# Optimization experiments

Measured on AMD Instinct MI355X. Metric: run time of the kernel, lower is better.

The kernel has to match this reference:

```python
import jax, jax.numpy as jnp
import numpy as np

NUM_BASES = 8


def setup_inputs() -> dict:
    key = jax.random.key(0)
    ks = jax.random.split(key, 8)
    N, E = 100000, 1600000
    IN_F, OUT_F, NUM_RELS = 128, 128, 16
    si = IN_F // NUM_BASES   # 16
    so = OUT_F // NUM_BASES  # 16
    return {
        "h": jax.random.normal(ks[0], (N, IN_F), dtype=jnp.float32),
        "norm": jax.random.uniform(ks[1], (N, 1), dtype=jnp.float32),
        "edge_src": jax.random.randint(ks[2], (E,), 0, N, dtype=jnp.int32),
        "edge_dst": jax.random.randint(ks[3], (E,), 0, N, dtype=jnp.int32),
        "edge_type": jax.random.randint(ks[4], (E,), 0, NUM_RELS, dtype=jnp.int32),
        "weight": jax.random.normal(ks[5], (NUM_RELS, NUM_BASES * si * so), dtype=jnp.float32) * 0.1,
        "bias_param": jax.random.normal(ks[6], (OUT_F,), dtype=jnp.float32) * 0.1,
        "loop_weight": jax.random.normal(ks[7], (IN_F, OUT_F), dtype=jnp.float32) * 0.1,
    }


def reference(h, norm, edge_src, edge_dst, edge_type, weight, bias_param, loop_weight):
    N, in_feat = h.shape
    out_feat = loop_weight.shape[1]
    si = in_feat // NUM_BASES
    so = out_feat // NUM_BASES
    E = edge_type.shape[0]

    # self-loop message (dropout=0.0 -> identity)
    loop_message = h @ loop_weight                      # [N, out_feat]

    # msg_func: gather per-edge relation weight blocks and do block-diag bmm
    W = weight[edge_type].reshape(E, NUM_BASES, si, so)  # [E, B, si, so]
    src = h[edge_src].reshape(E, NUM_BASES, si)          # [E, B, si]
    msg = jnp.einsum("ebi,ebio->ebo", src, W).reshape(E, out_feat)

    # scatter-sum messages to destination nodes, rescale by norm
    agg = jax.ops.segment_sum(msg, edge_dst, num_segments=N)  # [N, out_feat]
    node_repr = agg * norm

    # bias + self-loop + activation
    node_repr = node_repr + bias_param + loop_message
    return jax.nn.relu(node_repr)
```

## Files before the change

kernel.cpp:

```cpp
#include <hip/hip_runtime.h>


__global__ __launch_bounds__(256) void rgcn_init_kernel(
    const float* __restrict__ h, const float* __restrict__ loop_w,
    const float* __restrict__ bias, float* __restrict__ out, int N) {
  __shared__ float lw[128 * 128];
  for (int idx = threadIdx.x; idx < 128 * 128 / 4; idx += 256) {
    ((float4*)lw)[idx] = ((const float4*)loop_w)[idx];
  }
  __syncthreads();

  const int lane = threadIdx.x & 63;
  const int wid = threadIdx.x >> 6;
  const int group0 = blockIdx.x * 4 + wid;
  const int ngroups = gridDim.x * 4;
  const int totgroups = (N + 3) >> 2;
  const float b0 = bias[lane];
  const float b1 = bias[64 + lane];

  for (int g = group0; g < totgroups; g += ngroups) {
    const int n0 = g * 4;
    const int nn = (N - n0 < 4) ? (N - n0) : 4;
    if (nn == 4) {
      const float* __restrict__ r0 = h + (size_t)n0 * 128;
      const float* __restrict__ r1 = r0 + 128;
      const float* __restrict__ r2 = r1 + 128;
      const float* __restrict__ r3 = r2 + 128;
      float a00 = b0, a01 = b1, a10 = b0, a11 = b1;
      float a20 = b0, a21 = b1, a30 = b0, a31 = b1;
#pragma unroll 4
      for (int k = 0; k < 128; ++k) {
        const float w0 = lw[k * 128 + lane];
        const float w1 = lw[k * 128 + 64 + lane];
        a00 = fmaf(r0[k], w0, a00); a01 = fmaf(r0[k], w1, a01);
        a10 = fmaf(r1[k], w0, a10); a11 = fmaf(r1[k], w1, a11);
        a20 = fmaf(r2[k], w0, a20); a21 = fmaf(r2[k], w1, a21);
        a30 = fmaf(r3[k], w0, a30); a31 = fmaf(r3[k], w1, a31);
      }
      float* __restrict__ o0 = out + (size_t)n0 * 128;
      o0[lane] = a00;        o0[64 + lane] = a01;
      o0[128 + lane] = a10;  o0[192 + lane] = a11;
      o0[256 + lane] = a20;  o0[320 + lane] = a21;
      o0[384 + lane] = a30;  o0[448 + lane] = a31;
    } else {
      for (int r = 0; r < nn; ++r) {
        const int n = n0 + r;
        const float* __restrict__ hr = h + (size_t)n * 128;
        float a0 = b0, a1 = b1;
#pragma unroll 4
        for (int k = 0; k < 128; ++k) {
          const float a = hr[k];
          a0 = fmaf(a, lw[k * 128 + lane], a0);
          a1 = fmaf(a, lw[k * 128 + 64 + lane], a1);
        }
        out[(size_t)n * 128 + lane] = a0;
        out[(size_t)n * 128 + 64 + lane] = a1;
      }
    }
  }
}

__global__ __launch_bounds__(256) void rgcn_edge_kernel(
    const float* __restrict__ h, const float* __restrict__ norm,
    const int* __restrict__ esrc, const int* __restrict__ edst,
    const int* __restrict__ etype, const float* __restrict__ weight,
    float* __restrict__ out, int E) {
  const int lane = threadIdx.x & 63;
  const int wid = threadIdx.x >> 6;
  const int wave0 = blockIdx.x * 4 + wid;
  const int nwaves = gridDim.x * 4;
  const int b = lane >> 4;
  const int o = lane & 15;

  for (int e = wave0; e < E; e += nwaves) {
    const int src = esrc[e];
    const int dst = edst[e];
    const int et = etype[e];

    const float s_lo = h[src * 128 + lane];
    const float s_hi = h[src * 128 + 64 + lane];
    const float nrm = norm[dst];

    const float* __restrict__ Wb = weight + et * 2048 + b * 256 + o;

    float m0 = 0.f, m1 = 0.f;
#pragma unroll
    for (int i = 0; i < 16; ++i) {
      const float a_lo = __shfl(s_lo, (lane & 48) + i, 64);
      const float a_hi = __shfl(s_hi, (lane & 48) + i, 64);
      m0 = fmaf(a_lo, Wb[i * 16], m0);
      m1 = fmaf(a_hi, Wb[1024 + i * 16], m1);
    }

    atomicAdd(&out[dst * 128 + lane], m0 * nrm);
    atomicAdd(&out[dst * 128 + 64 + lane], m1 * nrm);
  }
}

__global__ __launch_bounds__(256) void rgcn_relu_kernel(float* __restrict__ out,
                                                        int total4) {
  int i = blockIdx.x * 256 + threadIdx.x;
  const int stride = gridDim.x * 256;
  for (; i < total4; i += stride) {
    float4 v = ((float4*)out)[i];
    v.x = fmaxf(v.x, 0.f);
    v.y = fmaxf(v.y, 0.f);
    v.z = fmaxf(v.z, 0.f);
    v.w = fmaxf(v.w, 0.f);
    ((float4*)out)[i] = v;
  }
}

extern "C" void kernel_launch(void* const* d_in, const int* in_sizes, int n_in,
                              void* d_out, int out_size, void* d_ws, size_t ws_size,
                              hipStream_t stream) {
  const float* h      = (const float*)d_in[0];
  const float* norm   = (const float*)d_in[1];
  const int*   esrc   = (const int*)d_in[2];
  const int*   edst   = (const int*)d_in[3];
  const int*   etype  = (const int*)d_in[4];
  const float* weight = (const float*)d_in[5];
  const float* bias   = (const float*)d_in[6];
  const float* loop_w = (const float*)d_in[7];
  float* out = (float*)d_out;

  const int N = in_sizes[0] / 128;
  const int E = in_sizes[2];

  rgcn_init_kernel<<<2048, 256, 0, stream>>>(h, loop_w, bias, out, N);
  rgcn_edge_kernel<<<4096, 256, 0, stream>>>(h, norm, esrc, edst, etype, weight,
                                             out, E);
  rgcn_relu_kernel<<<2048, 256, 0, stream>>>(out, (N * 128) / 4);
}
```

Baseline: 927.8 us.

## Bucket edges by relation type and cache relation weights in registers per wave

Adds a counting-sort pipeline (histogram, scan, scatter) that groups edges by relation type into workspace buffers. A new edge kernel then gives each wave a contiguous chunk of sorted edges and reloads the 32 per-lane relation weights only when the type changes, replacing the shuffles with float4 loads of the source row. This cuts repeated weight gathers per edge at the cost of extra sort passes and 12 bytes of workspace traffic per edge. It falls back to the old kernel when the workspace is too small.

```diff
diff --git a/kernel.cpp b/kernel.cpp
--- a/kernel.cpp
+++ b/kernel.cpp
@@ -60,6 +60,121 @@
   }
 }
 
+__global__ void rgcn_zero_kernel(int* __restrict__ p) {
+  if (threadIdx.x < 32) p[threadIdx.x] = 0;
+}
+
+__global__ __launch_bounds__(256) void rgcn_hist_kernel(
+    const int* __restrict__ etype, int* __restrict__ ghist, int E) {
+  __shared__ int lh[16];
+  if (threadIdx.x < 16) lh[threadIdx.x] = 0;
+  __syncthreads();
+  for (int e = blockIdx.x * 256 + threadIdx.x; e < E; e += gridDim.x * 256)
+    atomicAdd(&lh[etype[e]], 1);
+  __syncthreads();
+  if (threadIdx.x < 16) atomicAdd(&ghist[threadIdx.x], lh[threadIdx.x]);
+}
+
+__global__ void rgcn_scan_kernel(const int* __restrict__ ghist,
+                                 int* __restrict__ cursor) {
+  if (threadIdx.x == 0) {
+    int run = 0;
+    for (int t = 0; t < 16; ++t) {
+      cursor[t] = run;
+      run += ghist[t];
+    }
+  }
+}
+
+__global__ __launch_bounds__(256) void rgcn_scatter_kernel(
+    const int* __restrict__ esrc, const int* __restrict__ edst,
+    const int* __restrict__ etype, int* __restrict__ cursor,
+    int* __restrict__ ssrc, int* __restrict__ sdst, int* __restrict__ stype,
+    int E, int EPB) {
+  __shared__ int lh[16];
+  __shared__ int lbase[16];
+  const int b0 = blockIdx.x * EPB;
+  const int b1 = min(E, b0 + EPB);
+  if (threadIdx.x < 16) lh[threadIdx.x] = 0;
+  __syncthreads();
+  for (int e = b0 + threadIdx.x; e < b1; e += 256) atomicAdd(&lh[etype[e]], 1);
+  __syncthreads();
+  if (threadIdx.x < 16) {
+    lbase[threadIdx.x] = atomicAdd(&cursor[threadIdx.x], lh[threadIdx.x]);
+    lh[threadIdx.x] = 0;
+  }
+  __syncthreads();
+  for (int e = b0 + threadIdx.x; e < b1; e += 256) {
+    const int t = etype[e];
+    const int r = atomicAdd(&lh[t], 1);
+    const int p = lbase[t] + r;
+    ssrc[p] = esrc[e];
+    sdst[p] = edst[e];
+    stype[p] = t;
+  }
+}
+
+__global__ __launch_bounds__(256) void rgcn_edge_sorted_kernel(
+    const float* __restrict__ h, const float* __restrict__ norm,
+    const int* __restrict__ ssrc, const int* __restrict__ sdst,
+    const int* __restrict__ stype, const float* __restrict__ weight,
+    float* __restrict__ out, int E, int chunk) {
+  const int lane = threadIdx.x & 63;
+  const int wid = blockIdx.x * 4 + (threadIdx.x >> 6);
+  const int b = lane >> 4;
+  const int o = lane & 15;
+
+  long e0 = (long)wid * chunk;
+  if (e0 >= E) return;
+  long e1 = e0 + chunk;
+  if (e1 > E) e1 = E;
+
+  int cur = -1;
+  float wlo[16], whi[16];
+
+  for (long e = e0; e < e1; ++e) {
+    const int t = stype[e];
+    if (t != cur) {
+      cur = t;
+      const float* __restrict__ wb = weight + t * 2048 + b * 256 + o;
+#pragma unroll
+      for (int i = 0; i < 16; ++i) {
+        wlo[i] = wb[i * 16];
+        whi[i] = wb[1024 + i * 16];
+      }
+    }
+    const int src = ssrc[e];
+    const int dst = sdst[e];
+    const float nrm = norm[dst];
+
+    const float4* __restrict__ hp =
+        (const float4*)(h + (size_t)src * 128) + b * 4;
+    const float4 x0 = hp[0], x1 = hp[1], x2 = hp[2], x3 = hp[3];
+    const float4 y0 = hp[16], y1 = hp[17], y2 = hp[18], y3 = hp[19];
+
+    float a0 = x0.x * wlo[0], a1 = x0.y * wlo[1];
+    a0 = fmaf(x0.z, wlo[2], a0);  a1 = fmaf(x0.w, wlo[3], a1);
+    a0 = fmaf(x1.x, wlo[4], a0);  a1 = fmaf(x1.y, wlo[5], a1);
+    a0 = fmaf(x1.z, wlo[6], a0);  a1 = fmaf(x1.w, wlo[7], a1);
+    a0 = fmaf(x2.x, wlo[8], a0);  a1 = fmaf(x2.y, wlo[9], a1);
+    a0 = fmaf(x2.z, wlo[10], a0); a1 = fmaf(x2.w, wlo[11], a1);
+    a0 = fmaf(x3.x, wlo[12], a0); a1 = fmaf(x3.y, wlo[13], a1);
+    a0 = fmaf(x3.z, wlo[14], a0); a1 = fmaf(x3.w, wlo[15], a1);
+
+    float c0 = y0.x * whi[0], c1 = y0.y * whi[1];
+    c0 = fmaf(y0.z, whi[2], c0);  c1 = fmaf(y0.w, whi[3], c1);
+    c0 = fmaf(y1.x, whi[4], c0);  c1 = fmaf(y1.y, whi[5], c1);
+    c0 = fmaf(y1.z, whi[6], c0);  c1 = fmaf(y1.w, whi[7], c1);
+    c0 = fmaf(y2.x, whi[8], c0);  c1 = fmaf(y2.y, whi[9], c1);
+    c0 = fmaf(y2.z, whi[10], c0); c1 = fmaf(y2.w, whi[11], c1);
+    c0 = fmaf(y3.x, whi[12], c0); c1 = fmaf(y3.y, whi[13], c1);
+    c0 = fmaf(y3.z, whi[14], c0); c1 = fmaf(y3.w, whi[15], c1);
+
+    atomicAdd(&out[(size_t)dst * 128 + lane], (a0 + a1) * nrm);
+    atomicAdd(&out[(size_t)dst * 128 + 64 + lane], (c0 + c1) * nrm);
+  }
+}
+
 __global__ __launch_bounds__(256) void rgcn_edge_kernel(
     const float* __restrict__ h, const float* __restrict__ norm,
     const int* __restrict__ esrc, const int* __restrict__ edst,
@@ -76,13 +191,10 @@
     const int src = esrc[e];
     const int dst = edst[e];
     const int et = etype[e];
-
     const float s_lo = h[src * 128 + lane];
     const float s_hi = h[src * 128 + 64 + lane];
     const float nrm = norm[dst];
-
     const float* __restrict__ Wb = weight + et * 2048 + b * 256 + o;
-
     float m0 = 0.f, m1 = 0.f;
 #pragma unroll
     for (int i = 0; i < 16; ++i) {
@@ -91,7 +203,6 @@
       m0 = fmaf(a_lo, Wb[i * 16], m0);
       m1 = fmaf(a_hi, Wb[1024 + i * 16], m1);
     }
-
     atomicAdd(&out[dst * 128 + lane], m0 * nrm);
     atomicAdd(&out[dst * 128 + 64 + lane], m1 * nrm);
   }
@@ -128,7 +239,30 @@
   const int E = in_sizes[2];
 
   rgcn_init_kernel<<<2048, 256, 0, stream>>>(h, loop_w, bias, out, N);
-  rgcn_edge_kernel<<<4096, 256, 0, stream>>>(h, norm, esrc, edst, etype, weight,
-                                             out, E);
+
+  const size_t need = 256 + 12ull * (size_t)E;
+  if (ws_size >= need) {
+    int* ghist  = (int*)d_ws;
+    int* cursor = ghist + 16;
+    int* ssrc   = ghist + 64;
+    int* sdst   = ssrc + E;
+    int* stype  = sdst + E;
+
+    rgcn_zero_kernel<<<1, 64, 0, stream>>>(ghist);
+    rgcn_hist_kernel<<<1024, 256, 0, stream>>>(etype, ghist, E);
+    rgcn_scan_kernel<<<1, 64, 0, stream>>>(ghist, cursor);
+    const int EPB = 4096;
+    rgcn_scatter_kernel<<<(E + EPB - 1) / EPB, 256, 0, stream>>>(
+        esrc, edst, etype, cursor, ssrc, sdst, stype, E, EPB);
+
+    const int nwaves = 4096 * 4;
+    const int chunk = (E + nwaves - 1) / nwaves;
+    rgcn_edge_sorted_kernel<<<4096, 256, 0, stream>>>(
+        h, norm, ssrc, sdst, stype, weight, out, E, chunk);
+  } else {
+    rgcn_edge_kernel<<<4096, 256, 0, stream>>>(h, norm, esrc, edst, etype,
+                                               weight, out, E);
+  }
+
   rgcn_relu_kernel<<<2048, 256, 0, stream>>>(out, (N * 128) / 4);
 }
```

Result: slower. 1.034 ms (+11.5%).

## Bucket edges by destination range and relation, accumulate messages in LDS

Applied to the files above, without the earlier changes.

Adds a counting-sort preprocessing step (histogram, scan, scatter) that groups edges by 64-node destination range and relation type. The new edge kernel then keeps one relation's weight block in registers per wave, accumulates messages in shared memory with LDS atomics, and applies the norm, the ReLU and the combine with the self-loop output in one pass. This removes the global float atomics and the per-edge weight gather, and fuses away the ReLU kernel. In exchange it adds several extra launches, a single-block scan and workspace use, and the per-bin work may be unbalanced across waves.

```diff
diff --git a/kernel.cpp b/kernel.cpp
--- a/kernel.cpp
+++ b/kernel.cpp
@@ -1,5 +1,8 @@
 #include <hip/hip_runtime.h>
 
+
+#define RANGE_BITS 6
+#define RANGE (1 << RANGE_BITS)
 
 __global__ __launch_bounds__(256) void rgcn_init_kernel(
     const float* __restrict__ h, const float* __restrict__ loop_w,
@@ -60,6 +63,143 @@
   }
 }
 
+__global__ __launch_bounds__(256) void rgcn_zero_kernel(int* __restrict__ p,
+                                                        int n) {
+  for (int i = blockIdx.x * 256 + threadIdx.x; i < n; i += gridDim.x * 256)
+    p[i] = 0;
+}
+
+__global__ __launch_bounds__(256) void rgcn_hist_kernel(
+    const int* __restrict__ edst, const int* __restrict__ etype,
+    int* __restrict__ cnt, int E) {
+  for (int e = blockIdx.x * 256 + threadIdx.x; e < E; e += gridDim.x * 256) {
+    const int bin = ((edst[e] >> RANGE_BITS) << 4) + etype[e];
+    atomicAdd(&cnt[bin], 1);
+  }
+}
+
+__global__ __launch_bounds__(1024) void rgcn_scan_kernel(
+    const int* __restrict__ cnt, int* __restrict__ bin_ptr,
+    int* __restrict__ cursor, int bins) {
+  __shared__ int part[1024];
+  const int t = threadIdx.x;
+  const int chunk = (bins + 1023) >> 10;
+  const int lo = t * chunk;
+  const int hi = min(bins, lo + chunk);
+  int s = 0;
+  for (int i = lo; i < hi; ++i) s += cnt[i];
+  part[t] = s;
+  __syncthreads();
+#pragma unroll
+  for (int off = 1; off < 1024; off <<= 1) {
+    const int add = (t >= off) ? part[t - off] : 0;
+    __syncthreads();
+    part[t] += add;
+    __syncthreads();
+  }
+  int run = (t == 0) ? 0 : part[t - 1];
+  for (int i = lo; i < hi; ++i) {
+    const int c = cnt[i];
+    bin_ptr[i] = run;
+    cursor[i] = run;
+    run += c;
+  }
+  if (t == 1023) bin_ptr[bins] = part[1023];
+}
+
+__global__ __launch_bounds__(256) void rgcn_scatter_kernel(
+    const int* __restrict__ esrc, const int* __restrict__ edst,
+    const int* __restrict__ etype, int* __restrict__ cursor,
+    int* __restrict__ srec, int E) {
+  for (int e = blockIdx.x * 256 + threadIdx.x; e < E; e += gridDim.x * 256) {
+    const int d = edst[e];
+    const int bin = ((d >> RANGE_BITS) << 4) + etype[e];
+    const int p = atomicAdd(&cursor[bin], 1);
+    srec[p] = (esrc[e] << RANGE_BITS) | (d & (RANGE - 1));
+  }
+}
+
+__global__ __launch_bounds__(512) void rgcn_edge_lds_kernel(
+    const float* __restrict__ h, const float* __restrict__ norm,
+    const int* __restrict__ srec, const int* __restrict__ bin_ptr,
+    const float* __restrict__ weight, float* __restrict__ out, int N) {
+  __shared__ float acc[RANGE * 128];
+  for (int idx = threadIdx.x; idx < RANGE * 128 / 4; idx += 512)
+    ((float4*)acc)[idx] = make_float4(0.f, 0.f, 0.f, 0.f);
+  __syncthreads();
+
+  const int lane = threadIdx.x & 63;
+  const int w = threadIdx.x >> 6;
+  const int b = lane >> 4;
+  const int o = lane & 15;
+  const int r = blockIdx.x;
+
+  for (int tt = 0; tt < 2; ++tt) {
+    const int t = w * 2 + tt;
+    const int e0 = bin_ptr[r * 16 + t];
+    const int e1 = bin_ptr[r * 16 + t + 1];
+    if (e0 == e1) continue;
+
+    const float* __restrict__ wb = weight + t * 2048 + b * 256 + o;
+    float wlo[16], whi[16];
+#pragma unroll
+    for (int i = 0; i < 16; ++i) {
+      wlo[i] = wb[i * 16];
+      whi[i] = wb[1024 + i * 16];
+    }
+
+#pragma unroll 2
+    for (int e = e0; e < e1; ++e) {
+      const int rec = srec[e];
+      const int src = rec >> RANGE_BITS;
+      const int dl = rec & (RANGE - 1);
+
+      const float4* __restrict__ hp =
+          (const float4*)(h + (size_t)src * 128) + (b << 2);
+      const float4 x0 = hp[0], x1 = hp[1], x2 = hp[2], x3 = hp[3];
+      const float4 y0 = hp[16], y1 = hp[17], y2 = hp[18], y3 = hp[19];
+
+      float a0 = x0.x * wlo[0], a1 = x0.y * wlo[1];
+      a0 = fmaf(x0.z, wlo[2], a0);  a1 = fmaf(x0.w, wlo[3], a1);
+      a0 = fmaf(x1.x, wlo[4], a0);  a1 = fmaf(x1.y, wlo[5], a1);
+      a0 = fmaf(x1.z, wlo[6], a0);  a1 = fmaf(x1.w, wlo[7], a1);
+      a0 = fmaf(x2.x, wlo[8], a0);  a1 = fmaf(x2.y, wlo[9], a1);
+      a0 = fmaf(x2.z, wlo[10], a0); a1 = fmaf(x2.w, wlo[11], a1);
+      a0 = fmaf(x3.x, wlo[12], a0); a1 = fmaf(x3.y, wlo[13], a1);
+      a0 = fmaf(x3.z, wlo[14], a0); a1 = fmaf(x3.w, wlo[15], a1);
+
+      float c0 = y0.x * whi[0], c1 = y0.y * whi[1];
+      c0 = fmaf(y0.z, whi[2], c0);  c1 = fmaf(y0.w, whi[3], c1);
+      c0 = fmaf(y1.x, whi[4], c0);  c1 = fmaf(y1.y, whi[5], c1);
+      c0 = fmaf(y1.z, whi[6], c0);  c1 = fmaf(y1.w, whi[7], c1);
+      c0 = fmaf(y2.x, whi[8], c0);  c1 = fmaf(y2.y, whi[9], c1);
+      c0 = fmaf(y2.z, whi[10], c0); c1 = fmaf(y2.w, whi[11], c1);
+      c0 = fmaf(y3.x, whi[12], c0); c1 = fmaf(y3.y, whi[13], c1);
+      c0 = fmaf(y3.z, whi[14], c0); c1 = fmaf(y3.w, whi[15], c1);
+
+      atomicAdd(&acc[dl * 128 + lane], a0 + a1);
+      atomicAdd(&acc[dl * 128 + 64 + lane], c0 + c1);
+    }
+  }
+  __syncthreads();
+
+  for (int idx = threadIdx.x; idx < RANGE * 32; idx += 512) {
+    const int dl = idx >> 5;
+    const int c4 = idx & 31;
+    const int d = (r << RANGE_BITS) + dl;
+    if (d < N) {
+      const float nm = norm[d];
+      const float4 a = ((const float4*)acc)[idx];
+      float4 ov = ((float4*)out)[d * 32 + c4];
+      ov.x = fmaxf(fmaf(a.x, nm, ov.x), 0.f);
+      ov.y = fmaxf(fmaf(a.y, nm, ov.y), 0.f);
+      ov.z = fmaxf(fmaf(a.z, nm, ov.z), 0.f);
+      ov.w = fmaxf(fmaf(a.w, nm, ov.w), 0.f);
+      ((float4*)out)[d * 32 + c4] = ov;
+    }
+  }
+}
+
 __global__ __launch_bounds__(256) void rgcn_edge_kernel(
     const float* __restrict__ h, const float* __restrict__ norm,
     const int* __restrict__ esrc, const int* __restrict__ edst,
@@ -76,13 +216,10 @@
     const int src = esrc[e];
     const int dst = edst[e];
     const int et = etype[e];
-
     const float s_lo = h[src * 128 + lane];
     const float s_hi = h[src * 128 + 64 + lane];
     const float nrm = norm[dst];
-
     const float* __restrict__ Wb = weight + et * 2048 + b * 256 + o;
-
     float m0 = 0.f, m1 = 0.f;
 #pragma unroll
     for (int i = 0; i < 16; ++i) {
@@ -91,7 +228,6 @@
       m0 = fmaf(a_lo, Wb[i * 16], m0);
       m1 = fmaf(a_hi, Wb[1024 + i * 16], m1);
     }
-
     atomicAdd(&out[dst * 128 + lane], m0 * nrm);
     atomicAdd(&out[dst * 128 + 64 + lane], m1 * nrm);
   }
@@ -126,9 +262,30 @@
 
   const int N = in_sizes[0] / 128;
   const int E = in_sizes[2];
+  const int nrels = in_sizes[5] / 2048;
 
   rgcn_init_kernel<<<2048, 256, 0, stream>>>(h, loop_w, bias, out, N);
-  rgcn_edge_kernel<<<4096, 256, 0, stream>>>(h, norm, esrc, edst, etype, weight,
-                                             out, E);
-  rgcn_relu_kernel<<<2048, 256, 0, stream>>>(out, (N * 128) / 4);
-}
+
+  const int nRanges = (N + RANGE - 1) >> RANGE_BITS;
+  const int bins = nRanges * 16;
+  const size_t need = ((size_t)(3 * bins + 8) + (size_t)E) * 4;
+
+  if (nrels == 16 && N < (1 << 25) && ws_size >= need) {
+    int* cnt     = (int*)d_ws;
+    int* bin_ptr = cnt + bins;
+    int* cursor  = bin_ptr + bins + 4;
+    int* srec    = cursor + bins;
+
+    rgcn_zero_kernel<<<64, 256, 0, stream>>>(cnt, bins);
+    rgcn_hist_kernel<<<1024, 256, 0, stream>>>(edst, etype, cnt, E);
+    rgcn_scan_kernel<<<1, 1024, 0, stream>>>(cnt, bin_ptr, cursor, bins);
+    rgcn_scatter_kernel<<<2048, 256, 0, stream>>>(esrc, edst, etype, cursor,
+                                                  srec, E);
+    rgcn_edge_lds_kernel<<<nRanges, 512, 0, stream>>>(h, norm, srec, bin_ptr,
+                                                      weight, out, N);
+  } else {
+    rgcn_edge_kernel<<<4096, 256, 0, stream>>>(h, norm, esrc, edst, etype,
+                                               weight, out, E);
+    rgcn_relu_kernel<<<2048, 256, 0, stream>>>(out, (N * 128) / 4);
+  }
+}
```

Result: slower. 1.529 ms (+64.8%).

## Replace atomic edge scatter with CSR build and per-destination gather

Applied to the files above, without the earlier changes.

Builds a destination-sorted CSR on device each call (histogram, single-block scan, atomic scatter of packed src/type records), then runs a gather kernel with one wave per destination node that accumulates messages in registers and fuses norm, the self-loop add and ReLU. This removes the per-edge float atomics on the output and the separate ReLU pass. The weight is transposed so each lane reads contiguous float4 rows. The cost is several extra launches, a serial single-block scan over 100k bins, and integer atomics during the scatter.

```diff
diff --git a/kernel.cpp b/kernel.cpp
--- a/kernel.cpp
+++ b/kernel.cpp
@@ -60,6 +60,127 @@
   }
 }
 
+__global__ __launch_bounds__(256) void rgcn_transpose_w_kernel(
+    const float* __restrict__ weight, float* __restrict__ wT, int total) {
+  for (int idx = blockIdx.x * 256 + threadIdx.x; idx < total;
+       idx += gridDim.x * 256) {
+    const int t = idx >> 11;
+    const int r = idx & 2047;
+    const int bb = r >> 8;
+    const int i = (r >> 4) & 15;
+    const int o = r & 15;
+    wT[t * 2048 + bb * 256 + o * 16 + i] = weight[idx];
+  }
+}
+
+__global__ __launch_bounds__(256) void rgcn_zero_kernel(int* __restrict__ p,
+                                                        int n) {
+  for (int i = blockIdx.x * 256 + threadIdx.x; i < n; i += gridDim.x * 256)
+    p[i] = 0;
+}
+
+__global__ __launch_bounds__(256) void rgcn_hist_kernel(
+    const int* __restrict__ edst, int* __restrict__ cnt, int E) {
+  for (int e = blockIdx.x * 256 + threadIdx.x; e < E; e += gridDim.x * 256)
+    atomicAdd(&cnt[edst[e]], 1);
+}
+
+__global__ __launch_bounds__(1024) void rgcn_scan_kernel(
+    const int* __restrict__ cnt, int* __restrict__ row_ptr,
+    int* __restrict__ cursor, int bins) {
+  __shared__ int part[1024];
+  const int t = threadIdx.x;
+  const int chunk = (bins + 1023) >> 10;
+  const int lo = t * chunk;
+  const int hi = min(bins, lo + chunk);
+  int s = 0;
+  for (int i = lo; i < hi; ++i) s += cnt[i];
+  part[t] = s;
+  __syncthreads();
+#pragma unroll
+  for (int off = 1; off < 1024; off <<= 1) {
+    const int add = (t >= off) ? part[t - off] : 0;
+    __syncthreads();
+    part[t] += add;
+    __syncthreads();
+  }
+  int run = (t == 0) ? 0 : part[t - 1];
+  for (int i = lo; i < hi; ++i) {
+    const int c = cnt[i];
+    row_ptr[i] = run;
+    cursor[i] = run;
+    run += c;
+  }
+  if (t == 1023) row_ptr[bins] = part[1023];
+}
+
+__global__ __launch_bounds__(256) void rgcn_scatter_kernel(
+    const int* __restrict__ esrc, const int* __restrict__ edst,
+    const int* __restrict__ etype, int* __restrict__ cursor,
+    int* __restrict__ srec, int E) {
+  for (int e = blockIdx.x * 256 + threadIdx.x; e < E; e += gridDim.x * 256) {
+    const int d = edst[e];
+    const int p = atomicAdd(&cursor[d], 1);
+    srec[p] = (esrc[e] << 4) | etype[e];
+  }
+}
+
+__global__ __launch_bounds__(256) void rgcn_gather_kernel(
+    const float* __restrict__ h, const float* __restrict__ norm,
+    const int* __restrict__ srec, const int* __restrict__ row_ptr,
+    const float* __restrict__ wT, float* __restrict__ out, int N) {
+  const int lane = threadIdx.x & 63;
+  const int d = blockIdx.x * 4 + (threadIdx.x >> 6);
+  if (d >= N) return;
+  const int b = lane >> 4;
+  const int o = lane & 15;
+
+  const int e0 = row_ptr[d];
+  const int e1 = row_ptr[d + 1];
+
+  float acc0 = 0.f, acc1 = 0.f;
+
+#pragma unroll 2
+  for (int e = e0; e < e1; ++e) {
+    const int rec = srec[e];
+    const int src = rec >> 4;
+    const int t = rec & 15;
+
+    const float4* __restrict__ hp =
+        (const float4*)(h + (size_t)src * 128) + (b << 2);
+    const float4* __restrict__ wp =
+        (const float4*)(wT + t * 2048 + b * 256 + (o << 4));
+
+    const float4 x0 = hp[0], x1 = hp[1], x2 = hp[2], x3 = hp[3];
+    const float4 y0 = hp[16], y1 = hp[17], y2 = hp[18], y3 = hp[19];
+    const float4 w0 = wp[0], w1 = wp[1], w2 = wp[2], w3 = wp[3];
+    const float4 v0 = wp[256], v1 = wp[257], v2 = wp[258], v3 = wp[259];
+
+    acc0 = fmaf(x0.x, w0.x, acc0); acc0 = fmaf(x0.y, w0.y, acc0);
+    acc0 = fmaf(x0.z, w0.z, acc0); acc0 = fmaf(x0.w, w0.w, acc0);
+    acc0 = fmaf(x1.x, w1.x, acc0); acc0 = fmaf(x1.y, w1.y, acc0);
+    acc0 = fmaf(x1.z, w1.z, acc0); acc0 = fmaf(x1.w, w1.w, acc0);
+    acc0 = fmaf(x2.x, w2.x, acc0); acc0 = fmaf(x2.y, w2.y, acc0);
+    acc0 = fmaf(x2.z, w2.z, acc0); acc0 = fmaf(x2.w, w2.w, acc0);
+    acc0 = fmaf(x3.x, w3.x, acc0); acc0 = fmaf(x3.y, w3.y, acc0);
+    acc0 = fmaf(x3.z, w3.z, acc0); acc0 = fmaf(x3.w, w3.w, acc0);
+
+    acc1 = fmaf(y0.x, v0.x, acc1); acc1 = fmaf(y0.y, v0.y, acc1);
+    acc1 = fmaf(y0.z, v0.z, acc1); acc1 = fmaf(y0.w, v0.w, acc1);
+    acc1 = fmaf(y1.x, v1.x, acc1); acc1 = fmaf(y1.y, v1.y, acc1);
+    acc1 = fmaf(y1.z, v1.z, acc1); acc1 = fmaf(y1.w, v1.w, acc1);
+    acc1 = fmaf(y2.x, v2.x, acc1); acc1 = fmaf(y2.y, v2.y, acc1);
+    acc1 = fmaf(y2.z, v2.z, acc1); acc1 = fmaf(y2.w, v2.w, acc1);
+    acc1 = fmaf(y3.x, v3.x, acc1); acc1 = fmaf(y3.y, v3.y, acc1);
+    acc1 = fmaf(y3.z, v3.z, acc1); acc1 = fmaf(y3.w, v3.w, acc1);
+  }
+
+  const float nm = norm[d];
+  const size_t base = (size_t)d * 128;
+  out[base + lane] = fmaxf(fmaf(acc0, nm, out[base + lane]), 0.f);
+  out[base + 64 + lane] = fmaxf(fmaf(acc1, nm, out[base + 64 + lane]), 0.f);
+}
+
 __global__ __launch_bounds__(256) void rgcn_edge_kernel(
     const float* __restrict__ h, const float* __restrict__ norm,
     const int* __restrict__ esrc, const int* __restrict__ edst,
@@ -76,13 +197,10 @@
     const int src = esrc[e];
     const int dst = edst[e];
     const int et = etype[e];
-
     const float s_lo = h[src * 128 + lane];
     const float s_hi = h[src * 128 + 64 + lane];
     const float nrm = norm[dst];
-
     const float* __restrict__ Wb = weight + et * 2048 + b * 256 + o;
-
     float m0 = 0.f, m1 = 0.f;
 #pragma unroll
     for (int i = 0; i < 16; ++i) {
@@ -91,7 +209,6 @@
       m0 = fmaf(a_lo, Wb[i * 16], m0);
       m1 = fmaf(a_hi, Wb[1024 + i * 16], m1);
     }
-
     atomicAdd(&out[dst * 128 + lane], m0 * nrm);
     atomicAdd(&out[dst * 128 + 64 + lane], m1 * nrm);
   }
@@ -126,9 +243,37 @@
 
   const int N = in_sizes[0] / 128;
   const int E = in_sizes[2];
+  const int nrels = in_sizes[5] / 2048;
+  const int wtotal = in_sizes[5];
 
   rgcn_init_kernel<<<2048, 256, 0, stream>>>(h, loop_w, bias, out, N);
-  rgcn_edge_kernel<<<4096, 256, 0, stream>>>(h, norm, esrc, edst, etype, weight,
-                                             out, E);
-  rgcn_relu_kernel<<<2048, 256, 0, stream>>>(out, (N * 128) / 4);
-}
+
+  size_t ofs_cnt = 0;
+  size_t ofs_rp = N;
+  size_t ofs_cur = (ofs_rp + N + 1 + 3) & ~(size_t)3;
+  size_t ofs_wT = (ofs_cur + N + 3) & ~(size_t)3;
+  size_t ofs_srec = ofs_wT + (size_t)wtotal;
+  const size_t need = (ofs_srec + (size_t)E) * 4;
+
+  if (nrels == 16 && N < (1 << 26) && ws_size >= need) {
+    int* base    = (int*)d_ws;
+    int* cnt     = base + ofs_cnt;
+    int* row_ptr = base + ofs_rp;
+    int* cursor  = base + ofs_cur;
+    float* wT    = (float*)(base + ofs_wT);
+    int* srec    = base + ofs_srec;
+
+    rgcn_transpose_w_kernel<<<32, 256, 0, stream>>>(weight, wT, wtotal);
+    rgcn_zero_kernel<<<128, 256, 0, stream>>>(cnt, N);
+    rgcn_hist_kernel<<<2048, 256, 0, stream>>>(edst, cnt, E);
+    rgcn_scan_kernel<<<1, 1024, 0, stream>>>(cnt, row_ptr, cursor, N);
+    rgcn_scatter_kernel<<<2048, 256, 0, stream>>>(esrc, edst, etype, cursor,
+                                                  srec, E);
+    rgcn_gather_kernel<<<(N + 3) / 4, 256, 0, stream>>>(h, norm, srec, row_ptr,
+                                                        wT, out, N);
+  } else {
+    rgcn_edge_kernel<<<4096, 256, 0, stream>>>(h, norm, esrc, edst, etype,
+                                               weight, out, E);
+    rgcn_relu_kernel<<<2048, 256, 0, stream>>>(out, (N * 128) / 4);
+  }
+}
```

Measured after the change: 1.598 ms. 72.2% more time.
